# Optimization experiments

Hardware: AMD Instinct MI355X
Metric: run time of the kernel (lower is better)

Reference implementation:

```python
import jax, jax.numpy as jnp
import numpy as np

N, D, M = 100000, 128, 2048


def setup_inputs() -> dict:
    key = jax.random.key(0)
    k1, k2, k3, k4 = jax.random.split(key, 4)
    X = jax.random.normal(k1, (N, D), dtype=jnp.float32)
    Y = jax.random.normal(k2, (N, 1), dtype=jnp.float32)
    centers = jax.random.normal(k3, (M, D), dtype=jnp.float32)
    # alpha is a buffer produced by an inner Falkon solve; use small random values
    alpha = jax.random.normal(k4, (M, 1), dtype=jnp.float32) * 0.01
    sigma = jnp.asarray(1.0, dtype=jnp.float32)     # Gaussian kernel lengthscale (nn.Parameter)
    penalty = jnp.asarray(5.0, dtype=jnp.float32)   # lambda = exp(-penalty)
    return {"X": X, "Y": Y, "centers": centers, "alpha": alpha,
            "sigma": sigma, "penalty": penalty}


def _rbf_mmv(A, B, v, sigma):
    # Gaussian (RBF) kernel mat-vec: exp(-||a-b||^2 / (2 sigma^2)) @ v
    # A:[n,d], B:[m,d], v:[m,1] -> [n,1]
    a2 = jnp.sum(A * A, axis=-1, keepdims=True)          # [n,1]
    b2 = jnp.sum(B * B, axis=-1, keepdims=True).T        # [1,m]
    sq = a2 + b2 - 2.0 * (A @ B.T)                       # [n,m] squared distances
    Kmat = jnp.exp(-sq / (2.0 * sigma * sigma))
    return Kmat @ v


def reference(X, Y, centers, alpha, sigma, penalty):
    # loss = mean((K_NM @ alpha - Y)^2) + exp(-penalty) * alpha^T K_MM alpha
    preds = _rbf_mmv(X, centers, alpha, sigma)                     # [N,1]
    loss = jnp.mean((preds - Y) ** 2)
    pen = jnp.exp(-penalty)
    reg = pen * (alpha.T @ _rbf_mmv(centers, centers, alpha, sigma))  # [1,1]
    total = loss + reg[0, 0]
    return total, preds
```

## Files before the change

### kernel.cpp

```cpp
#include <hip/hip_runtime.h>
#include <stdint.h>

typedef short short8 __attribute__((ext_vector_type(8)));
typedef float f32x4 __attribute__((ext_vector_type(4)));

#define TILE 128

__device__ __forceinline__ unsigned short f32_to_bf16(float f) {
    uint32_t u = __builtin_bit_cast(uint32_t, f);
    u += 0x7FFFu + ((u >> 16) & 1u);
    return (unsigned short)(u >> 16);
}
__device__ __forceinline__ float bf16_to_f32(unsigned short h) {
    return __builtin_bit_cast(float, (uint32_t)h << 16);
}

typedef const __attribute__((address_space(1))) uint32_t guint;
typedef __attribute__((address_space(3))) uint32_t luint;
__device__ __forceinline__ void dma16(const void* g, void* l) {
    __builtin_amdgcn_global_load_lds((guint*)g, (luint*)l, 16, 0, 0);
}

__global__ void prep_kernel(const float* __restrict__ C,
                            const float* __restrict__ alpha,
                            const float* __restrict__ sigma,
                            unsigned short* __restrict__ Bp,
                            float2* __restrict__ cw,
                            float* __restrict__ acc)
{
    const int t = threadIdx.x;
    const int g = blockIdx.x;
    const int r = t >> 4;
    const int c16 = t & 15;
    const int R = g * 16 + r;

    if (g == 0 && t == 0) {
        acc[0] = 0.f; acc[1] = 0.f;
        ((unsigned int*)acc)[2] = 0u;
    }

    const float4* src = (const float4*)(C + (size_t)R * 128 + c16 * 8);
    float4 va = src[0], vb = src[1];
    unsigned short h[8];
    h[0] = f32_to_bf16(va.x); h[1] = f32_to_bf16(va.y);
    h[2] = f32_to_bf16(va.z); h[3] = f32_to_bf16(va.w);
    h[4] = f32_to_bf16(vb.x); h[5] = f32_to_bf16(vb.y);
    h[6] = f32_to_bf16(vb.z); h[7] = f32_to_bf16(vb.w);
    float ss = 0.f;
    #pragma unroll
    for (int k = 0; k < 8; ++k) {
        float f = bf16_to_f32(h[k]);
        ss = fmaf(f, f, ss);
    }
    uint4 pk;
    pk.x = (uint32_t)h[0] | ((uint32_t)h[1] << 16);
    pk.y = (uint32_t)h[2] | ((uint32_t)h[3] << 16);
    pk.z = (uint32_t)h[4] | ((uint32_t)h[5] << 16);
    pk.w = (uint32_t)h[6] | ((uint32_t)h[7] << 16);
    *reinterpret_cast<uint4*>(Bp + (size_t)g * 2048 + c16 * 128 + r * 8) = pk;

    ss += __shfl_xor(ss, 1);
    ss += __shfl_xor(ss, 2);
    ss += __shfl_xor(ss, 4);
    ss += __shfl_xor(ss, 8);
    if (c16 == 0) {
        float sig = sigma[0];
        float q = 0.7213475204444817f / (sig * sig);
        cw[R] = make_float2(ss * q, alpha[R]);
    }
}

__global__ __launch_bounds__(512, 4)
void fused_kernel(const float* __restrict__ X, int N,
                  const float* __restrict__ Yv,
                  const unsigned short* __restrict__ Bp,
                  const float2* __restrict__ cw,
                  const float* __restrict__ alpha,
                  const float* __restrict__ sigma,
                  const float* __restrict__ penalty,
                  int nA, int nMt, int nBlk,
                  float* __restrict__ preds_out,
                  float* __restrict__ out0,
                  float* __restrict__ acc)
{
    __shared__ __align__(16) unsigned short ldsB[2][16384];
    __shared__ float a2p[TILE][4];
    __shared__ float predbuf[TILE][2];

    const int t    = threadIdx.x;
    const int lane = t & 63;
    const int wid  = t >> 6;
    const int wr   = wid >> 1;
    const int wc   = wid & 1;
    const int l15  = lane & 15;
    const int quad = lane >> 4;

    const float sig = sigma[0];
    const float q  = 0.7213475204444817f / (sig * sig);
    const float q2 = 2.0f * q;

    const bool regmode = (int)blockIdx.x >= nA;
    int rowbase;
    float rowterm[2][4];
    short8 a[8];

    if (!regmode) {
        rowbase = blockIdx.x * TILE;
        const int r_  = t >> 2;
        const int qtr = t & 3;
        const int grow = rowbase + r_;
        unsigned short* dstbase = &ldsB[0][0] + (r_ >> 4) * 2048 + (r_ & 15) * 8;
        float ss = 0.f;
        if (grow < N) {
            const float4* src = (const float4*)(X + (size_t)grow * 128 + qtr * 32);
            #pragma unroll
            for (int c = 0; c < 4; ++c) {
                float4 va = src[2 * c], vb = src[2 * c + 1];
                unsigned short h0 = f32_to_bf16(va.x), h1 = f32_to_bf16(va.y);
                unsigned short h2 = f32_to_bf16(va.z), h3 = f32_to_bf16(va.w);
                unsigned short h4 = f32_to_bf16(vb.x), h5 = f32_to_bf16(vb.y);
                unsigned short h6 = f32_to_bf16(vb.z), h7 = f32_to_bf16(vb.w);
                float f0 = bf16_to_f32(h0), f1 = bf16_to_f32(h1);
                float f2 = bf16_to_f32(h2), f3 = bf16_to_f32(h3);
                float f4 = bf16_to_f32(h4), f5 = bf16_to_f32(h5);
                float f6 = bf16_to_f32(h6), f7 = bf16_to_f32(h7);
                ss = fmaf(f0, f0, ss); ss = fmaf(f1, f1, ss);
                ss = fmaf(f2, f2, ss); ss = fmaf(f3, f3, ss);
                ss = fmaf(f4, f4, ss); ss = fmaf(f5, f5, ss);
                ss = fmaf(f6, f6, ss); ss = fmaf(f7, f7, ss);
                uint4 pk;
                pk.x = (uint32_t)h0 | ((uint32_t)h1 << 16);
                pk.y = (uint32_t)h2 | ((uint32_t)h3 << 16);
                pk.z = (uint32_t)h4 | ((uint32_t)h5 << 16);
                pk.w = (uint32_t)h6 | ((uint32_t)h7 << 16);
                *reinterpret_cast<uint4*>(dstbase + (qtr * 4 + c) * 128) = pk;
            }
        } else {
            uint4 z; z.x = z.y = z.z = z.w = 0u;
            #pragma unroll
            for (int c = 0; c < 4; ++c)
                *reinterpret_cast<uint4*>(dstbase + (qtr * 4 + c) * 128) = z;
        }
        a2p[r_][qtr] = ss;
        __syncthreads();
        #pragma unroll
        for (int i = 0; i < 2; ++i)
            #pragma unroll
            for (int r = 0; r < 4; ++r) {
                int rl = wr * 32 + i * 16 + quad * 4 + r;
                rowterm[i][r] = (a2p[rl][0] + a2p[rl][1] + a2p[rl][2] + a2p[rl][3]) * q;
            }
        const unsigned short* aLds = &ldsB[0][0] + (size_t)(wr * 2) * 2048 + lane * 8;
        #pragma unroll
        for (int i = 0; i < 2; ++i)
            #pragma unroll
            for (int kk = 0; kk < 4; ++kk)
                a[i * 4 + kk] = *reinterpret_cast<const short8*>(aLds + (size_t)i * 2048 + kk * 512);
        __syncthreads();
    } else {
        const int b2 = (int)blockIdx.x - nA;
        rowbase = b2 * TILE;
        const unsigned short* aG = Bp + (size_t)(b2 * 8 + wr * 2) * 2048 + lane * 8;
        #pragma unroll
        for (int i = 0; i < 2; ++i)
            #pragma unroll
            for (int kk = 0; kk < 4; ++kk)
                a[i * 4 + kk] = *reinterpret_cast<const short8*>(aG + (size_t)i * 2048 + kk * 512);
        #pragma unroll
        for (int i = 0; i < 2; ++i)
            #pragma unroll
            for (int r = 0; r < 4; ++r)
                rowterm[i][r] = cw[rowbase + wr * 32 + i * 16 + quad * 4 + r].x;
    }

    float srow[2][4] = {};
    const float2* cwb = cw + wc * 64 + l15;

    const int ldq = wid * 2048 + lane * 8;

    {
        const unsigned short* g = Bp + ldq;
        unsigned short* l = &ldsB[0][0] + ldq;
        #pragma unroll
        for (int k = 0; k < 4; ++k)
            dma16(g + k * 512, l + k * 512);
    }
    __syncthreads();

    for (int mt = 0; mt < nMt; ++mt) {
        if (mt + 1 < nMt) {
            const unsigned short* g = Bp + (size_t)(mt + 1) * 16384 + ldq;
            unsigned short* l = &ldsB[(mt + 1) & 1][0] + ldq;
            #pragma unroll
            for (int k = 0; k < 4; ++k)
                dma16(g + k * 512, l + k * 512);
        }

        float2 cj[4];
        #pragma unroll
        for (int j = 0; j < 4; ++j) cj[j] = cwb[(size_t)mt * 128 + j * 16];

        const unsigned short* bfr = &ldsB[mt & 1][0] + (size_t)(wc * 4) * 2048 + lane * 8;
        #pragma unroll
        for (int j = 0; j < 4; ++j) {
            short8 b[4];
            #pragma unroll
            for (int kk = 0; kk < 4; ++kk)
                b[kk] = *reinterpret_cast<const short8*>(bfr + (size_t)j * 2048 + kk * 512);

            f32x4 acc4[2];
            #pragma unroll
            for (int i = 0; i < 2; ++i) acc4[i] = (f32x4){0.f, 0.f, 0.f, 0.f};
            #pragma unroll
            for (int kk = 0; kk < 4; ++kk)
                #pragma unroll
                for (int i = 0; i < 2; ++i)
                    acc4[i] = __builtin_amdgcn_mfma_f32_16x16x32_bf16(
                        a[i * 4 + kk], b[kk], acc4[i], 0, 0, 0);

            #pragma unroll
            for (int i = 0; i < 2; ++i) {
                #pragma unroll
                for (int r = 0; r < 4; ++r) {
                    float u = fmaf(acc4[i][r], q2, -(rowterm[i][r] + cj[j].x));
                    float e = __builtin_amdgcn_exp2f(u);
                    srow[i][r] = fmaf(e, cj[j].y, srow[i][r]);
                }
            }
        }

        __syncthreads();
    }

    #pragma unroll
    for (int i = 0; i < 2; ++i) {
        #pragma unroll
        for (int r = 0; r < 4; ++r) {
            int rl = wr * 32 + i * 16 + quad * 4 + r;
            float v = srow[i][r];
            v += __shfl_xor(v, 1);
            v += __shfl_xor(v, 2);
            v += __shfl_xor(v, 4);
            v += __shfl_xor(v, 8);
            if (l15 == 0)
                predbuf[rl][wc] = v;
        }
    }
    __syncthreads();

    float contrib = 0.f;
    if (t < TILE) {
        int grow = rowbase + t;
        if (!regmode) {
            if (grow < N) {
                float pred = predbuf[t][0] + predbuf[t][1];
                preds_out[grow] = pred;
                float d = pred - Yv[grow];
                contrib = d * d;
            }
        } else {
            float pred = predbuf[t][0] + predbuf[t][1];
            contrib = alpha[grow] * pred;
        }
    }
    contrib += __shfl_xor(contrib, 1);
    contrib += __shfl_xor(contrib, 2);
    contrib += __shfl_xor(contrib, 4);
    contrib += __shfl_xor(contrib, 8);
    contrib += __shfl_xor(contrib, 16);
    contrib += __shfl_xor(contrib, 32);
    if (lane == 0 && wid < 2) atomicAdd(regmode ? (acc + 1) : (acc + 0), contrib);

    __syncthreads();
    if (t == 0) {
        __threadfence();
        unsigned int old = atomicAdd((unsigned int*)(acc + 2), 1u);
        if (old == (unsigned int)(nBlk - 1)) {
            float lv = atomicAdd(acc + 0, 0.0f);
            float rv = atomicAdd(acc + 1, 0.0f);
            out0[0] = lv / (float)N + __expf(-penalty[0]) * rv;
        }
    }
}

extern "C" void kernel_launch(void* const* d_in, const int* in_sizes, int n_in,
                              void* d_out, int out_size, void* d_ws, size_t ws_size,
                              hipStream_t stream) {
    const float* X       = (const float*)d_in[0];
    const float* Y       = (const float*)d_in[1];
    const float* centers = (const float*)d_in[2];
    const float* alpha   = (const float*)d_in[3];
    const float* sigma   = (const float*)d_in[4];
    const float* penalty = (const float*)d_in[5];
    float* out = (float*)d_out;

    const int N = in_sizes[1];
    const int M = in_sizes[3];

    unsigned short* Bp = (unsigned short*)d_ws;
    float2* cw = (float2*)((char*)d_ws + (size_t)M * 256);
    float* acc = (float*)((char*)d_ws + (size_t)M * 264);

    prep_kernel<<<M / 16, 256, 0, stream>>>(centers, alpha, sigma, Bp, cw, acc);

    const int nA  = (N + TILE - 1) / TILE;
    const int nMt = M / TILE;
    const int nBlk = nA + nMt;
    fused_kernel<<<nBlk, 512, 0, stream>>>(X, N, Y, Bp, cw, alpha, sigma, penalty,
                                           nA, nMt, nBlk, out + 1, out, acc);
}
```

Before: 182.7 us.

## Halve LDS stage size to raise occupancy and retune launch bounds

The double-buffered center tiles shrink from 128 to 64 centers per stage, halving LDS use. The X-tile staging buffer is aliased onto the same memory. The loop now runs twice as many stages, each with its own barrier, and loads the per-center weights inside the inner loop. Launch bounds are raised to 6 blocks per CU so more blocks can be resident and the tail of the grid shrinks. The cost is more synchronisation and prefetch steps, plus a risk of register pressure under the tighter bound.

```diff
diff --git a/kernel.cpp b/kernel.cpp
--- a/kernel.cpp
+++ b/kernel.cpp
@@ -70,7 +70,7 @@
     }
 }
 
-__global__ __launch_bounds__(512, 4)
+__global__ __launch_bounds__(512, 6)
 void fused_kernel(const float* __restrict__ X, int N,
                   const float* __restrict__ Yv,
                   const unsigned short* __restrict__ Bp,
@@ -83,9 +83,11 @@
                   float* __restrict__ out0,
                   float* __restrict__ acc)
 {
-    __shared__ __align__(16) unsigned short ldsB[2][16384];
+    __shared__ __align__(16) unsigned short ldsB[2][8192];
     __shared__ float a2p[TILE][4];
     __shared__ float predbuf[TILE][2];
+
+    unsigned short* uni = &ldsB[0][0];
 
     const int t    = threadIdx.x;
     const int lane = t & 63;
@@ -109,7 +111,7 @@
         const int r_  = t >> 2;
         const int qtr = t & 3;
         const int grow = rowbase + r_;
-        unsigned short* dstbase = &ldsB[0][0] + (r_ >> 4) * 2048 + (r_ & 15) * 8;
+        unsigned short* dstbase = uni + (r_ >> 4) * 2048 + (r_ & 15) * 8;
         float ss = 0.f;
         if (grow < N) {
             const float4* src = (const float4*)(X + (size_t)grow * 128 + qtr * 32);
@@ -150,7 +152,7 @@
                 int rl = wr * 32 + i * 16 + quad * 4 + r;
                 rowterm[i][r] = (a2p[rl][0] + a2p[rl][1] + a2p[rl][2] + a2p[rl][3]) * q;
             }
-        const unsigned short* aLds = &ldsB[0][0] + (size_t)(wr * 2) * 2048 + lane * 8;
+        const unsigned short* aLds = uni + (size_t)(wr * 2) * 2048 + lane * 8;
         #pragma unroll
         for (int i = 0; i < 2; ++i)
             #pragma unroll
@@ -174,35 +176,29 @@
     }
 
     float srow[2][4] = {};
-    const float2* cwb = cw + wc * 64 + l15;
-
-    const int ldq = wid * 2048 + lane * 8;
+
+    const int ldq = wid * 1024 + lane * 8;
+    const int nSt = nMt * 2;
 
     {
         const unsigned short* g = Bp + ldq;
         unsigned short* l = &ldsB[0][0] + ldq;
-        #pragma unroll
-        for (int k = 0; k < 4; ++k)
-            dma16(g + k * 512, l + k * 512);
+        dma16(g, l);
+        dma16(g + 512, l + 512);
     }
     __syncthreads();
 
-    for (int mt = 0; mt < nMt; ++mt) {
-        if (mt + 1 < nMt) {
-            const unsigned short* g = Bp + (size_t)(mt + 1) * 16384 + ldq;
-            unsigned short* l = &ldsB[(mt + 1) & 1][0] + ldq;
-            #pragma unroll
-            for (int k = 0; k < 4; ++k)
-                dma16(g + k * 512, l + k * 512);
-        }
-
-        float2 cj[4];
-        #pragma unroll
-        for (int j = 0; j < 4; ++j) cj[j] = cwb[(size_t)mt * 128 + j * 16];
-
-        const unsigned short* bfr = &ldsB[mt & 1][0] + (size_t)(wc * 4) * 2048 + lane * 8;
-        #pragma unroll
-        for (int j = 0; j < 4; ++j) {
+    for (int s = 0; s < nSt; ++s) {
+        if (s + 1 < nSt) {
+            const unsigned short* g = Bp + (size_t)(s + 1) * 8192 + ldq;
+            unsigned short* l = &ldsB[(s + 1) & 1][0] + ldq;
+            dma16(g, l);
+            dma16(g + 512, l + 512);
+        }
+
+        const unsigned short* bfr = &ldsB[s & 1][0] + (size_t)(wc * 4096) + lane * 8;
+        #pragma unroll
+        for (int j = 0; j < 2; ++j) {
             short8 b[4];
             #pragma unroll
             for (int kk = 0; kk < 4; ++kk)
@@ -218,13 +214,15 @@
                     acc4[i] = __builtin_amdgcn_mfma_f32_16x16x32_bf16(
                         a[i * 4 + kk], b[kk], acc4[i], 0, 0, 0);
 
+            float2 cj = cw[(size_t)s * 64 + wc * 32 + j * 16 + l15];
+
             #pragma unroll
             for (int i = 0; i < 2; ++i) {
                 #pragma unroll
                 for (int r = 0; r < 4; ++r) {
-                    float u = fmaf(acc4[i][r], q2, -(rowterm[i][r] + cj[j].x));
+                    float u = fmaf(acc4[i][r], q2, -(rowterm[i][r] + cj.x));
                     float e = __builtin_amdgcn_exp2f(u);
-                    srow[i][r] = fmaf(e, cj[j].y, srow[i][r]);
+                    srow[i][r] = fmaf(e, cj.y, srow[i][r]);
                 }
             }
         }
```

Result: no change. 185.0 us (+1.2%).
